# Kernel tuning notes

Measured on AMD Instinct MI355X. Metric: run time of the kernel, lower is better.

Reference implementation:

```python
import jax, jax.numpy as jnp
import numpy as np

N_NODES = 50000
N_EDGES = 800000
IN_C = 128
HID = 64
HEADS = 4
OUT_C = 32
NEG_SLOPE = 0.2
EPS = 1e-16


def _gat_conv(x, edge_index, W, att_src, att_dst, bias, heads, out_c, concat):
    # PyG GATConv (eval mode, add_self_loops=True).
    N = x.shape[0]
    # append self loops
    loops = jnp.arange(N, dtype=edge_index.dtype)
    src = jnp.concatenate([edge_index[0], loops])
    dst = jnp.concatenate([edge_index[1], loops])
    h = (x @ W).reshape(N, heads, out_c)                      # [N,H,C]
    a_src = jnp.sum(h * att_src, axis=-1)                     # [N,H]
    a_dst = jnp.sum(h * att_dst, axis=-1)                     # [N,H]
    alpha = a_src[src] + a_dst[dst]                           # [E,H]
    alpha = jnp.where(alpha >= 0, alpha, NEG_SLOPE * alpha)   # leaky_relu
    amax = jax.ops.segment_max(alpha, dst, num_segments=N)    # [N,H]
    ex = jnp.exp(alpha - amax[dst])
    denom = jax.ops.segment_sum(ex, dst, num_segments=N)      # [N,H]
    coef = ex / (denom[dst] + EPS)                            # [E,H]
    msg = h[src] * coef[:, :, None]                           # [E,H,C]
    out = jax.ops.segment_sum(msg, dst, num_segments=N)       # [N,H,C]
    if concat:
        out = out.reshape(N, heads * out_c)
    else:
        out = out.mean(axis=1)
    return out + bias


def setup_inputs() -> dict:
    key = jax.random.key(0)
    ks = jax.random.split(key, 12)
    x = jax.random.normal(ks[0], (N_NODES, IN_C), dtype=jnp.float32)
    edge_index = jax.random.randint(ks[1], (2, N_EDGES), 0, N_NODES, dtype=jnp.int64)
    s1 = 1.0 / np.sqrt(IN_C)
    s2 = 1.0 / np.sqrt(HID * HEADS)
    W1 = jax.random.uniform(ks[2], (IN_C, HEADS * HID), jnp.float32, -s1, s1)
    att_src1 = jax.random.uniform(ks[3], (HEADS, HID), jnp.float32, -s1, s1)
    att_dst1 = jax.random.uniform(ks[4], (HEADS, HID), jnp.float32, -s1, s1)
    b1 = jnp.zeros((HEADS * HID,), jnp.float32)
    W2 = jax.random.uniform(ks[5], (HEADS * HID, OUT_C), jnp.float32, -s2, s2)
    att_src2 = jax.random.uniform(ks[6], (1, OUT_C), jnp.float32, -s2, s2)
    att_dst2 = jax.random.uniform(ks[7], (1, OUT_C), jnp.float32, -s2, s2)
    b2 = jnp.zeros((OUT_C,), jnp.float32)
    return {"x": x, "edge_index": edge_index, "W1": W1, "att_src1": att_src1,
            "att_dst1": att_dst1, "b1": b1, "W2": W2, "att_src2": att_src2,
            "att_dst2": att_dst2, "b2": b2}


def reference(x, edge_index, W1, att_src1, att_dst1, b1, W2, att_src2, att_dst2, b2):
    h = _gat_conv(x, edge_index, W1, att_src1, att_dst1, b1, HEADS, HID, concat=True)
    h = jax.nn.elu(h)
    out = _gat_conv(h, edge_index, W2, att_src2, att_dst2, b2, 1, OUT_C, concat=False)
    return out
```

## Files before the change

### kernel.cpp

```cpp
#include <hip/hip_runtime.h>

#define NN 50000
#define NE 800000
#define ETOT 850000
#define INC 128
#define HIDC 64
#define HEADS 4
#define C1 256
#define OUTC 32
#define NEG 0.2f
#define EPSV 1e-16f
#define SLOT_CAP 56

#define NB_CASTX 3125
#define NB_ZERO  196
#define NB_W1T   128
#define NB_W2T   32
#define NB_PREP  (NB_CASTX + NB_ZERO + NB_W1T + NB_W2T)
#define EB       3321
#define NB_G1S   782
#define NB_G1    (NB_G1S * 4)
#define NB_GS    (EB + NB_G1)

#define CURS  0
#define ASRC1 50000
#define ADST1 250000
#define ASRC2 450000
#define ADST2 500000
#define SLOTS 550000
#define W1T   3350000
#define W2T   3366384
#define XBF   3370480
#define H1B   6570480
#define H2B   12970480
#define H3OFF 19370480
#define WS_NEED_FLOATS 20970480ull

typedef __attribute__((ext_vector_type(8))) short short8v;
typedef __attribute__((ext_vector_type(4))) float floatx4;

__device__ __forceinline__ unsigned short f2bf(float f) {
    unsigned u = __float_as_uint(f);
    unsigned r = (u + 0x7fffu + ((u >> 16) & 1u)) >> 16;
    return (unsigned short)r;
}
__device__ __forceinline__ float bf2f(unsigned short s) {
    return __uint_as_float(((unsigned)s) << 16);
}
__device__ __forceinline__ float lrelu(float v) { return v >= 0.f ? v : NEG * v; }

__global__ __launch_bounds__(256) void prep(const float* __restrict__ x,
                                            const float* __restrict__ W1,
                                            const float* __restrict__ W2,
                                            unsigned short* __restrict__ xbf,
                                            unsigned short* __restrict__ w1t,
                                            unsigned short* __restrict__ w2t,
                                            int* __restrict__ curs) {
    const int bid = blockIdx.x, tid = threadIdx.x;
    if (bid < NB_CASTX) {
        int i = bid * 256 + tid;
        float4 v0 = ((const float4*)x)[i * 2];
        float4 v1 = ((const float4*)x)[i * 2 + 1];
        short8v o;
        o[0] = (short)f2bf(v0.x); o[1] = (short)f2bf(v0.y);
        o[2] = (short)f2bf(v0.z); o[3] = (short)f2bf(v0.w);
        o[4] = (short)f2bf(v1.x); o[5] = (short)f2bf(v1.y);
        o[6] = (short)f2bf(v1.z); o[7] = (short)f2bf(v1.w);
        *(short8v*)(xbf + (size_t)i * 8) = o;
    } else if (bid < NB_CASTX + NB_ZERO) {
        int i = (bid - NB_CASTX) * 256 + tid;
        if (i < NN) curs[i] = 0;
    } else if (bid < NB_CASTX + NB_ZERO + NB_W1T) {
        int i = (bid - NB_CASTX - NB_ZERO) * 256 + tid;
        int n = i >> 7, k = i & 127;
        w1t[(size_t)n * INC + k] = f2bf(W1[(size_t)k * C1 + n]);
    } else {
        int i = (bid - NB_CASTX - NB_ZERO - NB_W1T) * 256 + tid;
        int n = i >> 8, k = i & 255;
        w2t[(size_t)n * C1 + k] = f2bf(W2[(size_t)k * OUTC + n]);
    }
}

__global__ __launch_bounds__(256) void gemm1_scatter(const unsigned short* __restrict__ xbf,
                                                     const unsigned short* __restrict__ w1t,
                                                     const float* __restrict__ att_src,
                                                     const float* __restrict__ att_dst,
                                                     const int* __restrict__ ei,
                                                     unsigned short* __restrict__ h1b,
                                                     float* __restrict__ a_src,
                                                     float* __restrict__ a_dst,
                                                     int* __restrict__ curs,
                                                     int* __restrict__ slots) {
    const int bid = blockIdx.x;
    if (bid < EB) {
        int e = bid * 256 + threadIdx.x;
        if (e < ETOT) {
            int s, d;
            if (e < NE) { s = ei[e]; d = ei[NE + e]; }
            else { s = d = e - NE; }
            int pos = atomicAdd(&curs[d], 1);
            if (pos < SLOT_CAP) slots[(size_t)d * SLOT_CAP + pos] = s;
        }
        return;
    }
    const int b2 = bid - EB;
    const int strip = b2 % NB_G1S;
    const int by = b2 / NB_G1S;
    const int tid = threadIdx.x;
    const int w = tid >> 6, lane = tid & 63;
    const int l15 = lane & 15, kg = lane >> 4;
    const int mb = strip * 64 + w * 16;
    const int nb = by * 64;
    int ar = mb + l15; if (ar >= NN) ar = NN - 1;

    short8v a[4];
    #pragma unroll
    for (int ks = 0; ks < 4; ++ks)
        a[ks] = *(const short8v*)(xbf + (size_t)ar * INC + ks * 32 + kg * 8);

    short8v b[4][4];
    #pragma unroll
    for (int nt = 0; nt < 4; ++nt) {
        int nc = nb + nt * 16 + l15;
        #pragma unroll
        for (int ks = 0; ks < 4; ++ks)
            b[ks][nt] = *(const short8v*)(w1t + (size_t)nc * INC + ks * 32 + kg * 8);
    }

    floatx4 acc[4] = {{0.f,0.f,0.f,0.f},{0.f,0.f,0.f,0.f},{0.f,0.f,0.f,0.f},{0.f,0.f,0.f,0.f}};
    #pragma unroll
    for (int ks = 0; ks < 4; ++ks)
        #pragma unroll
        for (int nt = 0; nt < 4; ++nt)
            acc[nt] = __builtin_amdgcn_mfma_f32_16x16x32_bf16(a[ks], b[ks][nt], acc[nt], 0, 0, 0);

    #pragma unroll
    for (int nt = 0; nt < 4; ++nt)
        #pragma unroll
        for (int j = 0; j < 4; ++j) {
            int r = mb + kg * 4 + j;
            if (r < NN) h1b[(size_t)r * C1 + nb + nt * 16 + l15] = f2bf(acc[nt][j]);
        }

    float ws_[4], wd_[4];
    #pragma unroll
    for (int nt = 0; nt < 4; ++nt) {
        ws_[nt] = att_src[nb + nt * 16 + l15];
        wd_[nt] = att_dst[nb + nt * 16 + l15];
    }
    #pragma unroll
    for (int j = 0; j < 4; ++j) {
        float ps = acc[0][j] * ws_[0] + acc[1][j] * ws_[1] + acc[2][j] * ws_[2] + acc[3][j] * ws_[3];
        float pd = acc[0][j] * wd_[0] + acc[1][j] * wd_[1] + acc[2][j] * wd_[2] + acc[3][j] * wd_[3];
        #pragma unroll
        for (int m = 8; m; m >>= 1) {
            ps += __shfl_xor(ps, m);
            pd += __shfl_xor(pd, m);
        }
        int r = mb + kg * 4 + j;
        if (l15 == 0 && r < NN) {
            a_src[r * 4 + by] = ps;
            a_dst[r * 4 + by] = pd;
        }
    }
}

__global__ __launch_bounds__(256) void node1(const unsigned short* __restrict__ h1b,
                                             const int* __restrict__ curs,
                                             const int* __restrict__ slots,
                                             const float* __restrict__ a_src,
                                             const float* __restrict__ a_dst,
                                             const float* __restrict__ b1,
                                             unsigned short* __restrict__ h2b) {
    int wave = threadIdx.x >> 6, lane = threadIdx.x & 63;
    int n = blockIdx.x * 4 + wave;
    if (n >= NN) return;
    int h = lane >> 4;
    int cnt = curs[n]; if (cnt > SLOT_CAP) cnt = SLOT_CAP;
    const int* sl = slots + (size_t)n * SLOT_CAP;
    float adh = a_dst[n * 4 + h];
    float a0 = 0.f, a1 = 0.f, a2 = 0.f, a3 = 0.f, den = 0.f;
    int p = 0;
    for (; p + 7 < cnt; p += 8) {
        int sA[8];
        #pragma unroll
        for (int j = 0; j < 8; ++j) sA[j] = sl[p + j];
        uint2 rA[8];
        #pragma unroll
        for (int j = 0; j < 8; ++j) rA[j] = *(const uint2*)(h1b + (size_t)sA[j] * C1 + lane * 4);
        float eA[8];
        #pragma unroll
        for (int j = 0; j < 8; ++j) eA[j] = __expf(lrelu(a_src[sA[j] * 4 + h] + adh));
        #pragma unroll
        for (int j = 0; j < 8; ++j) {
            den += eA[j];
            a0 += bf2f((unsigned short)(rA[j].x & 0xffff)) * eA[j];
            a1 += bf2f((unsigned short)(rA[j].x >> 16)) * eA[j];
            a2 += bf2f((unsigned short)(rA[j].y & 0xffff)) * eA[j];
            a3 += bf2f((unsigned short)(rA[j].y >> 16)) * eA[j];
        }
    }
    for (; p + 3 < cnt; p += 4) {
        int sA[4];
        #pragma unroll
        for (int j = 0; j < 4; ++j) sA[j] = sl[p + j];
        uint2 rA[4];
        #pragma unroll
        for (int j = 0; j < 4; ++j) rA[j] = *(const uint2*)(h1b + (size_t)sA[j] * C1 + lane * 4);
        float eA[4];
        #pragma unroll
        for (int j = 0; j < 4; ++j) eA[j] = __expf(lrelu(a_src[sA[j] * 4 + h] + adh));
        #pragma unroll
        for (int j = 0; j < 4; ++j) {
            den += eA[j];
            a0 += bf2f((unsigned short)(rA[j].x & 0xffff)) * eA[j];
            a1 += bf2f((unsigned short)(rA[j].x >> 16)) * eA[j];
            a2 += bf2f((unsigned short)(rA[j].y & 0xffff)) * eA[j];
            a3 += bf2f((unsigned short)(rA[j].y >> 16)) * eA[j];
        }
    }
    for (; p < cnt; ++p) {
        int s = sl[p];
        float e = __expf(lrelu(a_src[s * 4 + h] + adh));
        den += e;
        uint2 rv = *(const uint2*)(h1b + (size_t)s * C1 + lane * 4);
        a0 += bf2f((unsigned short)(rv.x & 0xffff)) * e;
        a1 += bf2f((unsigned short)(rv.x >> 16)) * e;
        a2 += bf2f((unsigned short)(rv.y & 0xffff)) * e;
        a3 += bf2f((unsigned short)(rv.y >> 16)) * e;
    }
    float inv = 1.f / (den + EPSV);
    float4 bb = *(const float4*)(b1 + lane * 4);
    float o0 = a0 * inv + bb.x;
    float o1 = a1 * inv + bb.y;
    float o2 = a2 * inv + bb.z;
    float o3 = a3 * inv + bb.w;
    o0 = o0 > 0.f ? o0 : __expf(o0) - 1.f;
    o1 = o1 > 0.f ? o1 : __expf(o1) - 1.f;
    o2 = o2 > 0.f ? o2 : __expf(o2) - 1.f;
    o3 = o3 > 0.f ? o3 : __expf(o3) - 1.f;
    uint2 ov;
    ov.x = (unsigned)f2bf(o0) | ((unsigned)f2bf(o1) << 16);
    ov.y = (unsigned)f2bf(o2) | ((unsigned)f2bf(o3) << 16);
    *(uint2*)(h2b + (size_t)n * C1 + lane * 4) = ov;
}

__global__ __launch_bounds__(256) void gemm2_mfma(const unsigned short* __restrict__ h2b,
                                                  const unsigned short* __restrict__ w2t,
                                                  const float* __restrict__ att_src,
                                                  const float* __restrict__ att_dst,
                                                  float* __restrict__ h3,
                                                  float* __restrict__ a_src,
                                                  float* __restrict__ a_dst) {
    const int tid = threadIdx.x;
    const int w = tid >> 6, lane = tid & 63;
    const int l15 = lane & 15, kg = lane >> 4;
    const int mb = blockIdx.x * 64 + w * 16;
    int ar = mb + l15; if (ar >= NN) ar = NN - 1;

    short8v a[8];
    #pragma unroll
    for (int ks = 0; ks < 8; ++ks)
        a[ks] = *(const short8v*)(h2b + (size_t)ar * C1 + ks * 32 + kg * 8);

    short8v b[8][2];
    #pragma unroll
    for (int nt = 0; nt < 2; ++nt) {
        int nc = nt * 16 + l15;
        #pragma unroll
        for (int ks = 0; ks < 8; ++ks)
            b[ks][nt] = *(const short8v*)(w2t + (size_t)nc * C1 + ks * 32 + kg * 8);
    }

    floatx4 acc[2] = {{0.f,0.f,0.f,0.f},{0.f,0.f,0.f,0.f}};
    #pragma unroll
    for (int ks = 0; ks < 8; ++ks)
        #pragma unroll
        for (int nt = 0; nt < 2; ++nt)
            acc[nt] = __builtin_amdgcn_mfma_f32_16x16x32_bf16(a[ks], b[ks][nt], acc[nt], 0, 0, 0);

    #pragma unroll
    for (int nt = 0; nt < 2; ++nt)
        #pragma unroll
        for (int j = 0; j < 4; ++j) {
            int r = mb + kg * 4 + j;
            if (r < NN) h3[(size_t)r * OUTC + nt * 16 + l15] = acc[nt][j];
        }

    float ws0 = att_src[l15], ws1 = att_src[16 + l15];
    float wd0 = att_dst[l15], wd1 = att_dst[16 + l15];
    #pragma unroll
    for (int j = 0; j < 4; ++j) {
        float ps = acc[0][j] * ws0 + acc[1][j] * ws1;
        float pd = acc[0][j] * wd0 + acc[1][j] * wd1;
        #pragma unroll
        for (int m = 8; m; m >>= 1) {
            ps += __shfl_xor(ps, m);
            pd += __shfl_xor(pd, m);
        }
        int r = mb + kg * 4 + j;
        if (l15 == 0 && r < NN) {
            a_src[r] = ps;
            a_dst[r] = pd;
        }
    }
}

__global__ __launch_bounds__(256) void node2(const float* __restrict__ h3,
                                             const int* __restrict__ curs,
                                             const int* __restrict__ slots,
                                             const float* __restrict__ a_src,
                                             const float* __restrict__ a_dst,
                                             const float* __restrict__ b2,
                                             float* __restrict__ out) {
    int wave = threadIdx.x >> 6, lane = threadIdx.x & 63;
    int half = lane >> 5, c = lane & 31;
    int n = blockIdx.x * 8 + wave * 2 + half;
    if (n >= NN) return;
    int cnt = curs[n]; if (cnt > SLOT_CAP) cnt = SLOT_CAP;
    const int* sl = slots + (size_t)n * SLOT_CAP;
    float adn = a_dst[n];
    float acc = 0.f, den = 0.f;
    int p = 0;
    for (; p + 3 < cnt; p += 4) {
        int s0 = sl[p], s1 = sl[p + 1], s2 = sl[p + 2], s3 = sl[p + 3];
        float g0 = h3[(size_t)s0 * OUTC + c];
        float g1 = h3[(size_t)s1 * OUTC + c];
        float g2 = h3[(size_t)s2 * OUTC + c];
        float g3 = h3[(size_t)s3 * OUTC + c];
        float e0 = __expf(lrelu(a_src[s0] + adn));
        float e1 = __expf(lrelu(a_src[s1] + adn));
        float e2 = __expf(lrelu(a_src[s2] + adn));
        float e3 = __expf(lrelu(a_src[s3] + adn));
        den += e0 + e1 + e2 + e3;
        acc += g0 * e0 + g1 * e1 + g2 * e2 + g3 * e3;
    }
    for (; p < cnt; ++p) {
        int s = sl[p];
        float e = __expf(lrelu(a_src[s] + adn));
        den += e;
        acc += h3[(size_t)s * OUTC + c] * e;
    }
    out[(size_t)n * OUTC + c] = acc / (den + EPSV) + b2[c];
}

extern "C" void kernel_launch(void* const* d_in, const int* in_sizes, int n_in,
                              void* d_out, int out_size, void* d_ws, size_t ws_size,
                              hipStream_t stream) {
    if (ws_size < WS_NEED_FLOATS * 4ull) return;

    const float* x        = (const float*)d_in[0];
    const int* ei         = (const int*)d_in[1];
    const float* W1       = (const float*)d_in[2];
    const float* att_src1 = (const float*)d_in[3];
    const float* att_dst1 = (const float*)d_in[4];
    const float* b1       = (const float*)d_in[5];
    const float* W2       = (const float*)d_in[6];
    const float* att_src2 = (const float*)d_in[7];
    const float* att_dst2 = (const float*)d_in[8];
    const float* b2       = (const float*)d_in[9];
    float* out = (float*)d_out;
    float* ws  = (float*)d_ws;
    int*   wsi = (int*)d_ws;

    int*   curs   = wsi + CURS;
    float* a_src1 = ws + ASRC1;
    float* a_dst1 = ws + ADST1;
    float* a_src2 = ws + ASRC2;
    float* a_dst2 = ws + ADST2;
    int*   slots  = wsi + SLOTS;
    unsigned short* w1t = (unsigned short*)(ws + W1T);
    unsigned short* w2t = (unsigned short*)(ws + W2T);
    unsigned short* xbf = (unsigned short*)(ws + XBF);
    unsigned short* h1b = (unsigned short*)(ws + H1B);
    unsigned short* h2b = (unsigned short*)(ws + H2B);
    float* h3     = ws + H3OFF;

    hipLaunchKernelGGL(prep, dim3(NB_PREP), dim3(256), 0, stream,
                       x, W1, W2, xbf, w1t, w2t, curs);
    hipLaunchKernelGGL(gemm1_scatter, dim3(NB_GS), dim3(256), 0, stream,
                       xbf, w1t, att_src1, att_dst1, ei, h1b, a_src1, a_dst1, curs, slots);
    hipLaunchKernelGGL(node1, dim3((NN + 3) / 4), dim3(256), 0, stream,
                       h1b, curs, slots, a_src1, a_dst1, b1, h2b);
    hipLaunchKernelGGL(gemm2_mfma, dim3((NN + 63) / 64), dim3(256), 0, stream,
                       h2b, w2t, att_src2, att_dst2, h3, a_src2, a_dst2);
    hipLaunchKernelGGL(node2, dim3((NN + 7) / 8), dim3(256), 0, stream,
                       h3, curs, slots, a_src2, a_dst2, b2, out);
}
```

Baseline: 211.1 us.

## Move edge scatter into prep kernel with batched atomics, memset cursors

The edge-to-slot scatter moves from the GEMM1 kernel into the prep kernel. Each thread now handles 8 edges using vectorized int4 index loads and issues 8 independent atomics, and self-loops are handled in separate blocks. Cursor zeroing becomes a hipMemsetAsync, and GEMM1 runs as its own 2D-grid kernel. The aim is fewer scatter threads with more memory-level parallelism, so GEMM1 no longer shares a launch with atomic-heavy blocks. In exchange, the scatter can no longer overlap with GEMM1, and the memset adds an extra launch.

```diff
diff --git a/kernel.cpp b/kernel.cpp
--- a/kernel.cpp
+++ b/kernel.cpp
@@ -13,14 +13,16 @@
 #define SLOT_CAP 56
 
 #define NB_CASTX 3125
-#define NB_ZERO  196
 #define NB_W1T   128
 #define NB_W2T   32
-#define NB_PREP  (NB_CASTX + NB_ZERO + NB_W1T + NB_W2T)
-#define EB       3321
+#define NB_SCE   391
+#define NB_SCL   25
+#define OFF_W1T  NB_CASTX
+#define OFF_W2T  (OFF_W1T + NB_W1T)
+#define OFF_SCE  (OFF_W2T + NB_W2T)
+#define OFF_SCL  (OFF_SCE + NB_SCE)
+#define NB_PS    (OFF_SCL + NB_SCL)
 #define NB_G1S   782
-#define NB_G1    (NB_G1S * 4)
-#define NB_GS    (EB + NB_G1)
 
 #define CURS  0
 #define ASRC1 50000
@@ -49,13 +51,15 @@
 }
 __device__ __forceinline__ float lrelu(float v) { return v >= 0.f ? v : NEG * v; }
 
-__global__ __launch_bounds__(256) void prep(const float* __restrict__ x,
-                                            const float* __restrict__ W1,
-                                            const float* __restrict__ W2,
-                                            unsigned short* __restrict__ xbf,
-                                            unsigned short* __restrict__ w1t,
-                                            unsigned short* __restrict__ w2t,
-                                            int* __restrict__ curs) {
+__global__ __launch_bounds__(256) void prep_scatter(const float* __restrict__ x,
+                                                    const float* __restrict__ W1,
+                                                    const float* __restrict__ W2,
+                                                    const int* __restrict__ ei,
+                                                    unsigned short* __restrict__ xbf,
+                                                    unsigned short* __restrict__ w1t,
+                                                    unsigned short* __restrict__ w2t,
+                                                    int* __restrict__ curs,
+                                                    int* __restrict__ slots) {
     const int bid = blockIdx.x, tid = threadIdx.x;
     if (bid < NB_CASTX) {
         int i = bid * 256 + tid;
@@ -67,49 +71,60 @@
         o[4] = (short)f2bf(v1.x); o[5] = (short)f2bf(v1.y);
         o[6] = (short)f2bf(v1.z); o[7] = (short)f2bf(v1.w);
         *(short8v*)(xbf + (size_t)i * 8) = o;
-    } else if (bid < NB_CASTX + NB_ZERO) {
-        int i = (bid - NB_CASTX) * 256 + tid;
-        if (i < NN) curs[i] = 0;
-    } else if (bid < NB_CASTX + NB_ZERO + NB_W1T) {
-        int i = (bid - NB_CASTX - NB_ZERO) * 256 + tid;
+    } else if (bid < OFF_W2T) {
+        int i = (bid - OFF_W1T) * 256 + tid;
         int n = i >> 7, k = i & 127;
         w1t[(size_t)n * INC + k] = f2bf(W1[(size_t)k * C1 + n]);
-    } else {
-        int i = (bid - NB_CASTX - NB_ZERO - NB_W1T) * 256 + tid;
+    } else if (bid < OFF_SCE) {
+        int i = (bid - OFF_W2T) * 256 + tid;
         int n = i >> 8, k = i & 255;
         w2t[(size_t)n * C1 + k] = f2bf(W2[(size_t)k * OUTC + n]);
-    }
-}
-
-__global__ __launch_bounds__(256) void gemm1_scatter(const unsigned short* __restrict__ xbf,
-                                                     const unsigned short* __restrict__ w1t,
-                                                     const float* __restrict__ att_src,
-                                                     const float* __restrict__ att_dst,
-                                                     const int* __restrict__ ei,
-                                                     unsigned short* __restrict__ h1b,
-                                                     float* __restrict__ a_src,
-                                                     float* __restrict__ a_dst,
-                                                     int* __restrict__ curs,
-                                                     int* __restrict__ slots) {
-    const int bid = blockIdx.x;
-    if (bid < EB) {
-        int e = bid * 256 + threadIdx.x;
-        if (e < ETOT) {
-            int s, d;
-            if (e < NE) { s = ei[e]; d = ei[NE + e]; }
-            else { s = d = e - NE; }
-            int pos = atomicAdd(&curs[d], 1);
-            if (pos < SLOT_CAP) slots[(size_t)d * SLOT_CAP + pos] = s;
-        }
-        return;
-    }
-    const int b2 = bid - EB;
-    const int strip = b2 % NB_G1S;
-    const int by = b2 / NB_G1S;
+    } else if (bid < OFF_SCL) {
+        int t = (bid - OFF_SCE) * 256 + tid;
+        int e0 = t * 8;
+        if (e0 < NE) {
+            int4 s01 = *(const int4*)(ei + e0);
+            int4 s23 = *(const int4*)(ei + e0 + 4);
+            int4 d01 = *(const int4*)(ei + NE + e0);
+            int4 d23 = *(const int4*)(ei + NE + e0 + 4);
+            int ss[8] = {s01.x, s01.y, s01.z, s01.w, s23.x, s23.y, s23.z, s23.w};
+            int dd[8] = {d01.x, d01.y, d01.z, d01.w, d23.x, d23.y, d23.z, d23.w};
+            int pos[8];
+            #pragma unroll
+            for (int j = 0; j < 8; ++j) pos[j] = atomicAdd(&curs[dd[j]], 1);
+            #pragma unroll
+            for (int j = 0; j < 8; ++j)
+                if (pos[j] < SLOT_CAP) slots[(size_t)dd[j] * SLOT_CAP + pos[j]] = ss[j];
+        }
+    } else {
+        int t = (bid - OFF_SCL) * 256 + tid;
+        int base = t * 8;
+        int pos[8];
+        #pragma unroll
+        for (int j = 0; j < 8; ++j) {
+            int d = base + j;
+            pos[j] = (d < NN) ? atomicAdd(&curs[d], 1) : SLOT_CAP;
+        }
+        #pragma unroll
+        for (int j = 0; j < 8; ++j) {
+            int d = base + j;
+            if (d < NN && pos[j] < SLOT_CAP) slots[(size_t)d * SLOT_CAP + pos[j]] = d;
+        }
+    }
+}
+
+__global__ __launch_bounds__(256) void gemm1_mfma(const unsigned short* __restrict__ xbf,
+                                                  const unsigned short* __restrict__ w1t,
+                                                  const float* __restrict__ att_src,
+                                                  const float* __restrict__ att_dst,
+                                                  unsigned short* __restrict__ h1b,
+                                                  float* __restrict__ a_src,
+                                                  float* __restrict__ a_dst) {
     const int tid = threadIdx.x;
     const int w = tid >> 6, lane = tid & 63;
     const int l15 = lane & 15, kg = lane >> 4;
-    const int mb = strip * 64 + w * 16;
+    const int mb = blockIdx.x * 64 + w * 16;
+    const int by = blockIdx.y;
     const int nb = by * 64;
     int ar = mb + l15; if (ar >= NN) ar = NN - 1;
 
@@ -376,10 +391,11 @@
     unsigned short* h2b = (unsigned short*)(ws + H2B);
     float* h3     = ws + H3OFF;
 
-    hipLaunchKernelGGL(prep, dim3(NB_PREP), dim3(256), 0, stream,
-                       x, W1, W2, xbf, w1t, w2t, curs);
-    hipLaunchKernelGGL(gemm1_scatter, dim3(NB_GS), dim3(256), 0, stream,
-                       xbf, w1t, att_src1, att_dst1, ei, h1b, a_src1, a_dst1, curs, slots);
+    hipMemsetAsync(curs, 0, NN * sizeof(int), stream);
+    hipLaunchKernelGGL(prep_scatter, dim3(NB_PS), dim3(256), 0, stream,
+                       x, W1, W2, ei, xbf, w1t, w2t, curs, slots);
+    hipLaunchKernelGGL(gemm1_mfma, dim3(NB_G1S, 4), dim3(256), 0, stream,
+                       xbf, w1t, att_src1, att_dst1, h1b, a_src1, a_dst1);
     hipLaunchKernelGGL(node1, dim3((NN + 3) / 4), dim3(256), 0, stream,
                        h1b, curs, slots, a_src1, a_dst1, b1, h2b);
     hipLaunchKernelGGL(gemm2_mfma, dim3((NN + 63) / 64), dim3(256), 0, stream,
```

New measurement: 218.7 us. +3.6%, slower.
